# Performance work log

Measured on AMD Instinct MI355X. Metric: run time of the kernel, lower is better.

## Reference

```python
import jax, jax.numpy as jnp
import numpy as np

N, E = 50000, 800000
IN_FEAT = OUT_FEAT = 128
EMB = 3
K = 3  # k_order + 1
BN_EPS = 1e-5


def setup_inputs() -> dict:
    key = jax.random.key(0)
    ks = jax.random.split(key, 12)
    feature = jax.random.normal(ks[0], (N, IN_FEAT), jnp.float32)
    coords = jax.random.normal(ks[1], (N, EMB), jnp.float32)
    src = jax.random.randint(ks[2], (E,), 0, N, jnp.int32)
    dst = jax.random.randint(ks[3], (E,), 0, N, jnp.int32)
    order = jax.random.randint(ks[4], (E,), 0, K, jnp.int32)
    # xavier_normal_ on [K, in, out]: torch treats last two dims as (fan_in, fan_out)
    std_lin = float(np.sqrt(2.0 / (IN_FEAT + OUT_FEAT)))
    linear = jax.random.normal(ks[5], (K, IN_FEAT, OUT_FEAT), jnp.float32) * std_lin
    # attention_layer: Linear(EMB, OUT_FEAT, bias=False); store as [EMB, OUT_FEAT]
    lim_att = float(1.0 / np.sqrt(EMB))
    attW = jax.random.uniform(ks[6], (EMB, OUT_FEAT), jnp.float32, -lim_att, lim_att)
    lim_mlp = float(1.0 / np.sqrt(OUT_FEAT))
    mlp_w = jax.random.uniform(ks[7], (OUT_FEAT, OUT_FEAT), jnp.float32, -lim_mlp, lim_mlp)
    mlp_b = jax.random.uniform(ks[8], (OUT_FEAT,), jnp.float32, -lim_mlp, lim_mlp)
    bn_gamma = jnp.ones((OUT_FEAT,), jnp.float32)
    bn_beta = jnp.zeros((OUT_FEAT,), jnp.float32)
    return {"feature": feature, "coords": coords, "src": src, "dst": dst,
            "order": order, "linear": linear, "attW": attW,
            "mlp_w": mlp_w, "mlp_b": mlp_b, "bn_gamma": bn_gamma, "bn_beta": bn_beta}


def reference(feature, coords, src, dst, order, linear, attW, mlp_w, mlp_b, bn_gamma, bn_beta):
    n = feature.shape[0]
    # --- edge attention: dot(attention_layer(c_src - c_dst), h_src) ---
    dc = coords[src] - coords[dst]                      # [E, EMB]
    att = jnp.sum((dc @ attW) * feature[src], axis=1)   # [E]
    invdist = 1.0 / (jnp.sum(dc * dc, axis=1) + 1.0)    # [E], 1/(||dc||^2 + 1)
    # --- messages: per-edge weight selection linear[order] @ h_src ---
    # msg depends only on (src node, order): precompute per-order node transforms
    xk = jnp.einsum('ni,kio->kno', feature, linear)     # [K, N, OUT]
    msg = xk[order, src]                                # [E, OUT]
    # --- segment softmax over incoming edges of dst ---
    m = jax.ops.segment_max(att, dst, num_segments=n)   # [N]
    ex = jnp.exp(att - m[dst])                          # [E]
    denom = jax.ops.segment_sum(ex, dst, num_segments=n)
    d_g = denom[dst]
    alpha = ex / jnp.where(d_g > 0, d_g, 1.0)
    # --- weighted scatter-add aggregation ---
    w = (alpha * invdist)[:, None]                      # [E, 1]
    h = jax.ops.segment_sum(w * msg, dst, num_segments=n)  # [N, OUT]
    # --- mlp: Linear -> ReLU -> BatchNorm1d (training-mode batch stats) ---
    y = jax.nn.relu(h @ mlp_w.T + mlp_b)
    mean = jnp.mean(y, axis=0)
    var = jnp.var(y, axis=0)  # biased, matches torch BN normalization
    y = (y - mean) * jax.lax.rsqrt(var + BN_EPS) * bn_gamma + bn_beta
    return y
```

## Files before the change

kernel.cpp:

```cpp
#include <hip/hip_runtime.h>

#define N_NODES 50000
#define E_EDGES 800000
#define FEAT    128
#define KORD    3
#define BN_EPS  1e-5f
#define NB1     49
#define NBUK    49
#define BCAP    20480
#define NSHARD  16

typedef __fp16 f16x2 __attribute__((ext_vector_type(2)));
typedef __fp16 f16x8 __attribute__((ext_vector_type(8)));
typedef __attribute__((ext_vector_type(4))) float f32x4;

__device__ __forceinline__ unsigned h2u(f16x2 h) { union { f16x2 h; unsigned u; } c; c.h = h; return c.u; }
__device__ __forceinline__ f16x2 u2h(unsigned u) { union { unsigned u; f16x2 h; } c; c.u = u; return c.h; }

__device__ __forceinline__ void gload16(const void* g, void* l) {
    __builtin_amdgcn_global_load_lds(
        (const __attribute__((address_space(1))) unsigned int*)g,
        (__attribute__((address_space(3))) unsigned int*)l, 16, 0, 0);
}

__global__ void gprep(const float* __restrict__ W, const float* __restrict__ L,
                      __fp16* __restrict__ GT) {
    __shared__ float wrow[FEAT];
    const int o = blockIdx.x;
    const int i = threadIdx.x;
    wrow[i] = W[o * FEAT + i];
    __syncthreads();
    #pragma unroll
    for (int k = 0; k < KORD; ++k) {
        const float* lp = L + ((size_t)k * FEAT + i) * FEAT;
        float acc = 0.f;
        #pragma unroll 8
        for (int j = 0; j < FEAT; ++j) acc = fmaf(lp[j], wrow[j], acc);
        GT[(size_t)o * 384 + k * FEAT + i] = (__fp16)acc;
    }
}

__global__ void g_cast(const float* __restrict__ feat,
                       const float* __restrict__ coords,
                       const float* __restrict__ attW,
                       __fp16* __restrict__ fh,
                       float4* __restrict__ pk) {
    const int node = (blockIdx.x * blockDim.x + threadIdx.x) >> 6;
    const int lane = threadIdx.x & 63;
    if (node >= N_NODES) return;
    const float2 f = *(const float2*)(feat + (size_t)node * FEAT + lane * 2);
    *(f16x2*)(fh + (size_t)node * FEAT + lane * 2) = __builtin_amdgcn_cvt_pkrtz(f.x, f.y);
    float gg[3];
    #pragma unroll
    for (int j = 0; j < 3; ++j) {
        float p = f.x * attW[j * FEAT + lane * 2] + f.y * attW[j * FEAT + lane * 2 + 1];
        #pragma unroll
        for (int off = 32; off; off >>= 1) p += __shfl_xor(p, off);
        gg[j] = p;
    }
    if (lane == 0) {
        const float c0 = coords[node * 3 + 0], c1 = coords[node * 3 + 1], c2 = coords[node * 3 + 2];
        pk[2 * node]     = make_float4(c0, c1, c2, gg[0]);
        pk[2 * node + 1] = make_float4(gg[1], gg[2], 0.f, 0.f);
    }
}

__global__ __launch_bounds__(256)
void bucketA(const int* __restrict__ src, const int* __restrict__ dst,
             const int* __restrict__ order,
             int* __restrict__ cnt, int* __restrict__ gcur, int2* __restrict__ bbuf) {
    __shared__ int lcnt[NBUK];
    __shared__ int lbase[NBUK];
    const int tid = threadIdx.x;
    if (tid < NBUK) lcnt[tid] = 0;
    __syncthreads();
    const int e0 = blockIdx.x * 2048;
    int b[8], r[8], so[8], dd[8];
    #pragma unroll
    for (int i = 0; i < 8; ++i) {
        const int e = e0 + i * 256 + tid;
        if (e < E_EDGES) {
            dd[i] = dst[e];
            so[i] = (order[e] << 16) | src[e];
            b[i] = dd[i] >> 10;
            r[i] = atomicAdd(&lcnt[b[i]], 1);
            atomicAdd(cnt + dd[i], 1);
        } else b[i] = -1;
    }
    __syncthreads();
    if (tid < NBUK) lbase[tid] = atomicAdd(&gcur[tid], lcnt[tid]);
    __syncthreads();
    #pragma unroll
    for (int i = 0; i < 8; ++i)
        if (b[i] >= 0)
            bbuf[(size_t)b[i] * BCAP + lbase[b[i]] + r[i]] = make_int2(so[i], dd[i]);
}

__global__ __launch_bounds__(256)
void scan1(const int* __restrict__ cnt, int* __restrict__ rowptr, int* __restrict__ bsum) {
    __shared__ int lds[256];
    const int b = blockIdx.x, t = threadIdx.x;
    const int base = b * 1024 + t * 4;
    int v[4];
    #pragma unroll
    for (int i = 0; i < 4; ++i) v[i] = (base + i < N_NODES) ? cnt[base + i] : 0;
    lds[t] = v[0] + v[1] + v[2] + v[3];
    __syncthreads();
    for (int off = 1; off < 256; off <<= 1) {
        const int u = (t >= off) ? lds[t - off] : 0;
        __syncthreads();
        lds[t] += u;
        __syncthreads();
    }
    int excl = t ? lds[t - 1] : 0;
    if (t == 255) bsum[b] = lds[255];
    #pragma unroll
    for (int i = 0; i < 4; ++i) {
        if (base + i < N_NODES) rowptr[base + i] = excl;
        excl += v[i];
    }
}

__global__ void scan2(const int* __restrict__ bsum, int* __restrict__ boff,
                      int* __restrict__ rowptr) {
    const int lane = threadIdx.x;
    const int v = (lane < NB1) ? bsum[lane] : 0;
    int incl = v;
    #pragma unroll
    for (int off = 1; off < 64; off <<= 1) {
        const int u = __shfl_up(incl, off);
        if (lane >= off) incl += u;
    }
    if (lane < NB1) boff[lane] = incl - v;
    if (lane == 0) rowptr[N_NODES] = E_EDGES;
}

__global__ void scan3(int* __restrict__ rowptr, int* __restrict__ cursor,
                      const int* __restrict__ boff) {
    const int i = blockIdx.x * blockDim.x + threadIdx.x;
    if (i >= N_NODES) return;
    const int v = rowptr[i] + boff[i >> 10];
    rowptr[i] = v;
    cursor[i] = v;
}

__global__ void bucketB(const int* __restrict__ gcur, const int2* __restrict__ bbuf,
                        int* __restrict__ cursor, int* __restrict__ sord_p) {
    const int b = blockIdx.x >> 3;
    const int seg = blockIdx.x & 7;
    const int n = gcur[b];
    const int lo = (int)((long)n * seg / 8), hi = (int)((long)n * (seg + 1) / 8);
    for (int i = lo + (int)threadIdx.x; i < hi; i += 256) {
        const int2 ent = bbuf[(size_t)b * BCAP + i];
        const int pos = atomicAdd(cursor + ent.y, 1);
        sord_p[pos] = ent.x;
    }
}

__global__ void segagg(const float4* __restrict__ pk,
                       const int* __restrict__ sord_p,
                       const int* __restrict__ rowptr,
                       const __fp16* __restrict__ fh,
                       __fp16* __restrict__ agg) {
    __shared__ uint4 stash[4][72];
    const int node = (blockIdx.x * blockDim.x + threadIdx.x) >> 6;
    const int lane = threadIdx.x & 63;
    const int wid  = threadIdx.x >> 6;
    if (node >= N_NODES) return;
    const int beg = rowptr[node], end = rowptr[node + 1];
    const float4 b0 = pk[2 * node];

    if (lane < 8) stash[wid][64 + lane] = make_uint4(0u, 0u, 0u, 0u);

    float att0 = -1e30f, inv0 = 0.f; int sol0 = 0;
    float m = -1e30f, s = 0.f;
    int nch = 0;
    for (int cb = beg; cb < end; cb += 64, ++nch) {
        const int p = cb + lane;
        float a = -1e30f, iv = 0.f; int so = 0;
        if (p < end) {
            so = sord_p[p];
            const int sn = so & 0xFFFF;
            const float4 a0 = pk[2 * sn], a1 = pk[2 * sn + 1];
            const float dx = a0.x - b0.x, dy = a0.y - b0.y, dz = a0.z - b0.z;
            a = dx * a0.w + dy * a1.x + dz * a1.y;
            iv = 1.f / (dx * dx + dy * dy + dz * dz + 1.f);
        }
        if (nch == 0) { att0 = a; inv0 = iv; sol0 = so; }
        const float mn = fmaxf(m, a);
        s = s * __expf(m - mn) + ((p < end) ? __expf(a - mn) : 0.f);
        m = mn;
    }
    #pragma unroll
    for (int off = 32; off; off >>= 1) {
        const float mo = __shfl_xor(m, off), so_ = __shfl_xor(s, off);
        const float mn = fmaxf(m, mo);
        s = s * __expf(m - mn) + so_ * __expf(mo - mn);
        m = mn;
    }
    const float inv_s = s > 0.f ? 1.f / s : 0.f;

    const int grp = lane >> 4;
    const int fl  = lane & 15;
    f16x2 ac[3][4];
    #pragma unroll
    for (int o = 0; o < 3; ++o)
        #pragma unroll
        for (int q = 0; q < 4; ++q) ac[o][q] = (f16x2){0, 0};

    int ch = 0;
    for (int cb = beg; cb < end; cb += 64, ++ch) {
        const int p = cb + lane;
        float wl = 0.f; int so = 0;
        if (ch == 0) {
            wl = __expf(att0 - m) * inv_s * inv0;
            so = sol0;
        } else if (p < end) {
            so = sord_p[p];
            const int sn = so & 0xFFFF;
            const float4 a0 = pk[2 * sn], a1 = pk[2 * sn + 1];
            const float dx = a0.x - b0.x, dy = a0.y - b0.y, dz = a0.z - b0.z;
            const float a = dx * a0.w + dy * a1.x + dz * a1.y;
            wl = __expf(a - m) * inv_s / (dx * dx + dy * dy + dz * dz + 1.f);
        }
        const int k = so >> 16;
        const __fp16 wh = (__fp16)wl;
        f16x2 w2; w2.x = wh; w2.y = wh;
        const unsigned uw = h2u(w2);
        stash[wid][lane] = make_uint4(k == 0 ? uw : 0u, k == 1 ? uw : 0u,
                                      k == 2 ? uw : 0u, (unsigned)(so & 0xFFFF));
        const int ne = min(64, end - cb);
        const uint4* st = stash[wid];
        for (int t = 0; t < ne; t += 4) {
            const uint4 e = st[t + grp];
            const uint4 v = *(const uint4*)(fh + ((size_t)e.w << 7) + fl * 8);
            const f16x2 w0 = u2h(e.x), w1 = u2h(e.y), w2v = u2h(e.z);
            const f16x2 va = u2h(v.x), vb = u2h(v.y), vc = u2h(v.z), vd = u2h(v.w);
            ac[0][0] = __builtin_elementwise_fma(va, w0, ac[0][0]);
            ac[0][1] = __builtin_elementwise_fma(vb, w0, ac[0][1]);
            ac[0][2] = __builtin_elementwise_fma(vc, w0, ac[0][2]);
            ac[0][3] = __builtin_elementwise_fma(vd, w0, ac[0][3]);
            ac[1][0] = __builtin_elementwise_fma(va, w1, ac[1][0]);
            ac[1][1] = __builtin_elementwise_fma(vb, w1, ac[1][1]);
            ac[1][2] = __builtin_elementwise_fma(vc, w1, ac[1][2]);
            ac[1][3] = __builtin_elementwise_fma(vd, w1, ac[1][3]);
            ac[2][0] = __builtin_elementwise_fma(va, w2v, ac[2][0]);
            ac[2][1] = __builtin_elementwise_fma(vb, w2v, ac[2][1]);
            ac[2][2] = __builtin_elementwise_fma(vc, w2v, ac[2][2]);
            ac[2][3] = __builtin_elementwise_fma(vd, w2v, ac[2][3]);
        }
    }
    #pragma unroll
    for (int o = 0; o < 3; ++o)
        #pragma unroll
        for (int q = 0; q < 4; ++q) {
            ac[o][q] = ac[o][q] + u2h(__shfl_xor((int)h2u(ac[o][q]), 16));
            ac[o][q] = ac[o][q] + u2h(__shfl_xor((int)h2u(ac[o][q]), 32));
        }
    if (lane < 16) {
        __fp16* row = agg + (size_t)node * 384 + fl * 8;
        *(uint4*)(row)       = make_uint4(h2u(ac[0][0]), h2u(ac[0][1]), h2u(ac[0][2]), h2u(ac[0][3]));
        *(uint4*)(row + 128) = make_uint4(h2u(ac[1][0]), h2u(ac[1][1]), h2u(ac[1][2]), h2u(ac[1][3]));
        *(uint4*)(row + 256) = make_uint4(h2u(ac[2][0]), h2u(ac[2][1]), h2u(ac[2][2]), h2u(ac[2][3]));
    }
}

__global__ __launch_bounds__(256)
void mlp_gemm(const __fp16* __restrict__ agg, const __fp16* __restrict__ GT,
              float* __restrict__ out, int M,
              const float* __restrict__ bias, float* __restrict__ sbuf) {
    __shared__ char smem[49152];
    const int m0 = blockIdx.x * 64;
    const int tid = threadIdx.x;
    const int wave = tid >> 6, lane = tid & 63;
    const int wm0 = wave * 16;
    const int lrow = lane & 15;
    const int kg = lane >> 4;
    const int srow = lane >> 3;
    const int schunk = lane & 7;

    auto STAGE = [&](int buf, int kc) {
        char* base = smem + buf * 24576;
        #pragma unroll
        for (int j = 0; j < 2; ++j) {
            const int rl = wave * 16 + j * 8 + srow;
            const int rg = min(m0 + rl, M - 1);
            gload16(agg + (size_t)rg * 384 + kc * 64 + ((schunk ^ (rl & 7)) << 3),
                    base + (wave * 16 + j * 8) * 128);
        }
        #pragma unroll
        for (int j = 0; j < 4; ++j) {
            const int rl = wave * 32 + j * 8 + srow;
            gload16(GT + (size_t)rl * 384 + kc * 64 + ((schunk ^ (rl & 7)) << 3),
                    base + 8192 + (wave * 32 + j * 8) * 128);
        }
    };

    f32x4 acc[8];
    #pragma unroll
    for (int b = 0; b < 8; ++b) acc[b] = (f32x4){0.f, 0.f, 0.f, 0.f};

    STAGE(0, 0);
    __syncthreads();

    for (int kc = 0; kc < 6; ++kc) {
        const int buf = kc & 1;
        if (kc < 5) STAGE(buf ^ 1, kc + 1);
        const char* Ab = smem + buf * 24576;
        const char* Bb = Ab + 8192;
        f16x8 afr[2];
        #pragma unroll
        for (int ks = 0; ks < 2; ++ks) {
            const int row = wm0 + lrow;
            afr[ks] = *(const f16x8*)(Ab + row * 128 + (((ks * 4 + kg) ^ (row & 7)) << 4));
        }
        #pragma unroll
        for (int nf = 0; nf < 8; ++nf) {
            #pragma unroll
            for (int ks = 0; ks < 2; ++ks) {
                const int row = nf * 16 + lrow;
                f16x8 bfr = *(const f16x8*)(Bb + row * 128 + (((ks * 4 + kg) ^ (row & 7)) << 4));
                acc[nf] = __builtin_amdgcn_mfma_f32_16x16x32_f16(afr[ks], bfr, acc[nf], 0, 0, 0);
            }
        }
        __syncthreads();
    }

    float s[8], s2[8], bv[8];
    #pragma unroll
    for (int nf = 0; nf < 8; ++nf) { s[nf] = 0.f; s2[nf] = 0.f; bv[nf] = bias[nf * 16 + lrow]; }
    #pragma unroll
    for (int nf = 0; nf < 8; ++nf)
        #pragma unroll
        for (int rg = 0; rg < 4; ++rg) {
            const int row = m0 + wm0 + kg * 4 + rg;
            if (row < M) {
                const float v = fmaxf(acc[nf][rg] + bv[nf], 0.f);
                out[(size_t)row * FEAT + nf * 16 + lrow] = v;
                s[nf] += v;
                s2[nf] = fmaf(v, v, s2[nf]);
            }
        }
    #pragma unroll
    for (int nf = 0; nf < 8; ++nf) {
        s[nf]  += __shfl_xor(s[nf], 16);  s[nf]  += __shfl_xor(s[nf], 32);
        s2[nf] += __shfl_xor(s2[nf], 16); s2[nf] += __shfl_xor(s2[nf], 32);
    }
    __syncthreads();
    float* red = (float*)smem;
    if (lane < 16) {
        #pragma unroll
        for (int nf = 0; nf < 8; ++nf) {
            red[wave * 256 + nf * 16 + lane]       = s[nf];
            red[wave * 256 + 128 + nf * 16 + lane] = s2[nf];
        }
    }
    __syncthreads();
    if (tid < 128) {
        const float ss = red[tid] + red[256 + tid] + red[512 + tid] + red[768 + tid];
        const float qq = red[128 + tid] + red[384 + tid] + red[640 + tid] + red[896 + tid];
        float* sb = sbuf + (blockIdx.x & (NSHARD - 1)) * 256;
        atomicAdd(sb + tid, ss);
        atomicAdd(sb + FEAT + tid, qq);
    }
}

__global__ void normalize(float* __restrict__ y, const float* __restrict__ sbuf,
                          const float* __restrict__ gamma, const float* __restrict__ beta) {
    __shared__ float sc_s[FEAT], sh_s[FEAT];
    const int t = threadIdx.x;
    if (t < FEAT) {
        float ssum = 0.f, qsum = 0.f;
        #pragma unroll
        for (int sh = 0; sh < NSHARD; ++sh) {
            ssum += sbuf[sh * 256 + t];
            qsum += sbuf[sh * 256 + 128 + t];
        }
        const float mean = ssum / (float)N_NODES;
        const float var  = qsum / (float)N_NODES - mean * mean;
        const float sc   = gamma[t] * rsqrtf(var + BN_EPS);
        sc_s[t] = sc;
        sh_s[t] = beta[t] - mean * sc;
    }
    __syncthreads();
    const int idx = blockIdx.x * blockDim.x + t;
    const int o4 = (idx & 31) * 4;
    float4 v = *(float4*)(y + (size_t)idx * 4);
    const float4 sc = *(const float4*)(sc_s + o4);
    const float4 sh = *(const float4*)(sh_s + o4);
    v.x = fmaf(v.x, sc.x, sh.x);
    v.y = fmaf(v.y, sc.y, sh.y);
    v.z = fmaf(v.z, sc.z, sh.z);
    v.w = fmaf(v.w, sc.w, sh.w);
    *(float4*)(y + (size_t)idx * 4) = v;
}

extern "C" void kernel_launch(void* const* d_in, const int* in_sizes, int n_in,
                              void* d_out, int out_size, void* d_ws, size_t ws_size,
                              hipStream_t stream) {
    const float* feature = (const float*)d_in[0];
    const float* coords  = (const float*)d_in[1];
    const int*   src     = (const int*)d_in[2];
    const int*   dst     = (const int*)d_in[3];
    const int*   order   = (const int*)d_in[4];
    const float* linear  = (const float*)d_in[5];
    const float* attW    = (const float*)d_in[6];
    const float* mlp_w   = (const float*)d_in[7];
    const float* mlp_b   = (const float*)d_in[8];
    const float* gamma   = (const float*)d_in[9];
    const float* beta    = (const float*)d_in[10];
    float* out = (float*)d_out;

    char* p = (char*)d_ws;
    __fp16* fh           = (__fp16*)p;  p += (size_t)N_NODES * FEAT * 2;
    __fp16* agg          = (__fp16*)p;  p += (size_t)N_NODES * 384 * 2;
    __fp16* GT           = (__fp16*)p;  p += (size_t)FEAT * 384 * 2;
    float4* pk           = (float4*)p;  p += (size_t)N_NODES * 32;
    int*   sord_p        = (int*)p;     p += (size_t)E_EDGES * 4;
    int2*  bbuf          = (int2*)p;    p += (size_t)NBUK * BCAP * 8;
    int*   cnt           = (int*)p;     p += 200064;
    float* sbuf          = (float*)p;   p += NSHARD * 256 * 4;
    int*   gcur          = (int*)p;     p += 1024;
    int*   rowptr        = (int*)p;     p += 200064;
    int*   cursor        = (int*)p;     p += 200064;
    int*   bsum          = (int*)p;     p += 256;
    int*   boff          = (int*)p;     p += 256;

    hipMemsetAsync(cnt, 0, 200064 + NSHARD * 256 * 4 + 1024, stream);

    const int NWB = (N_NODES * 64) / 256;
    const int MB  = (N_NODES + 63) / 64;
    const int AB  = (E_EDGES + 2047) / 2048;

    gprep<<<FEAT, FEAT, 0, stream>>>(mlp_w, linear, GT);
    g_cast<<<NWB, 256, 0, stream>>>(feature, coords, attW, fh, pk);

    bucketA<<<AB, 256, 0, stream>>>(src, dst, order, cnt, gcur, bbuf);
    scan1<<<NB1, 256, 0, stream>>>(cnt, rowptr, bsum);
    scan2<<<1, 64, 0, stream>>>(bsum, boff, rowptr);
    scan3<<<(N_NODES + 255) / 256, 256, 0, stream>>>(rowptr, cursor, boff);
    bucketB<<<NBUK * 8, 256, 0, stream>>>(gcur, bbuf, cursor, sord_p);

    segagg<<<NWB, 256, 0, stream>>>(pk, sord_p, rowptr, fh, agg);

    mlp_gemm<<<MB, 256, 0, stream>>>(agg, GT, out, N_NODES, mlp_b, sbuf);
    normalize<<<(N_NODES * 32) / 256, 256, 0, stream>>>(out, sbuf, gamma, beta);
}
```

Measured before the change: 186.2 us.

## Precompute edge attention in bucket scatter, merge prep kernels, unroll gather loop

Moves the per-edge attention score and inverse-distance calculation from segagg into bucketB, which writes them to new CSR-ordered arrays att_p/invd_p. segagg then reads them contiguously instead of gathering node records twice. The gprep kernel is folded into extra blocks of g_cast, scan2 is folded into scan3 (each block recomputes the 49-entry prefix), and the feature-gather loop is unrolled by two to keep more loads in flight. This cuts two kernel launches and repeated random pk gathers, at the cost of extra global writes and reads of two 800K-float arrays and random-position scatter stores.

```diff
diff --git a/kernel.cpp b/kernel.cpp
--- a/kernel.cpp
+++ b/kernel.cpp
@@ -9,6 +9,7 @@
 #define NBUK    49
 #define BCAP    20480
 #define NSHARD  16
+#define NWB_BLKS 12500
 
 typedef __fp16 f16x2 __attribute__((ext_vector_type(2)));
 typedef __fp16 f16x8 __attribute__((ext_vector_type(8)));
@@ -23,28 +24,32 @@
         (__attribute__((address_space(3))) unsigned int*)l, 16, 0, 0);
 }
 
-__global__ void gprep(const float* __restrict__ W, const float* __restrict__ L,
-                      __fp16* __restrict__ GT) {
-    __shared__ float wrow[FEAT];
-    const int o = blockIdx.x;
-    const int i = threadIdx.x;
-    wrow[i] = W[o * FEAT + i];
-    __syncthreads();
-    #pragma unroll
-    for (int k = 0; k < KORD; ++k) {
-        const float* lp = L + ((size_t)k * FEAT + i) * FEAT;
-        float acc = 0.f;
-        #pragma unroll 8
-        for (int j = 0; j < FEAT; ++j) acc = fmaf(lp[j], wrow[j], acc);
-        GT[(size_t)o * 384 + k * FEAT + i] = (__fp16)acc;
-    }
-}
-
 __global__ void g_cast(const float* __restrict__ feat,
                        const float* __restrict__ coords,
                        const float* __restrict__ attW,
+                       const float* __restrict__ W,
+                       const float* __restrict__ L,
                        __fp16* __restrict__ fh,
-                       float4* __restrict__ pk) {
+                       float4* __restrict__ pk,
+                       __fp16* __restrict__ GT) {
+    __shared__ float wrow[FEAT];
+    if (blockIdx.x >= NWB_BLKS) {
+        const int o = blockIdx.x - NWB_BLKS;
+        const int i = threadIdx.x;
+        if (i < FEAT) wrow[i] = W[o * FEAT + i];
+        __syncthreads();
+        if (i < FEAT) {
+            #pragma unroll
+            for (int k = 0; k < KORD; ++k) {
+                const float* lp = L + ((size_t)k * FEAT + i) * FEAT;
+                float acc = 0.f;
+                #pragma unroll 8
+                for (int j = 0; j < FEAT; ++j) acc = fmaf(lp[j], wrow[j], acc);
+                GT[(size_t)o * 384 + k * FEAT + i] = (__fp16)acc;
+            }
+        }
+        return;
+    }
     const int node = (blockIdx.x * blockDim.x + threadIdx.x) >> 6;
     const int lane = threadIdx.x & 63;
     if (node >= N_NODES) return;
@@ -121,72 +126,73 @@
     }
 }
 
-__global__ void scan2(const int* __restrict__ bsum, int* __restrict__ boff,
-                      int* __restrict__ rowptr) {
-    const int lane = threadIdx.x;
-    const int v = (lane < NB1) ? bsum[lane] : 0;
-    int incl = v;
-    #pragma unroll
-    for (int off = 1; off < 64; off <<= 1) {
-        const int u = __shfl_up(incl, off);
-        if (lane >= off) incl += u;
-    }
-    if (lane < NB1) boff[lane] = incl - v;
-    if (lane == 0) rowptr[N_NODES] = E_EDGES;
-}
-
 __global__ void scan3(int* __restrict__ rowptr, int* __restrict__ cursor,
-                      const int* __restrict__ boff) {
-    const int i = blockIdx.x * blockDim.x + threadIdx.x;
-    if (i >= N_NODES) return;
-    const int v = rowptr[i] + boff[i >> 10];
-    rowptr[i] = v;
-    cursor[i] = v;
+                      const int* __restrict__ bsum) {
+    __shared__ int boff_s[64];
+    const int t = threadIdx.x;
+    if (t < 64) {
+        const int v = (t < NB1) ? bsum[t] : 0;
+        int incl = v;
+        #pragma unroll
+        for (int off = 1; off < 64; off <<= 1) {
+            const int u = __shfl_up(incl, off);
+            if (t >= off) incl += u;
+        }
+        boff_s[t] = incl - v;
+    }
+    __syncthreads();
+    const int i = blockIdx.x * 256 + t;
+    if (i < N_NODES) {
+        const int v = rowptr[i] + boff_s[i >> 10];
+        rowptr[i] = v;
+        cursor[i] = v;
+    }
+    if (i == 0) rowptr[N_NODES] = E_EDGES;
 }
 
 __global__ void bucketB(const int* __restrict__ gcur, const int2* __restrict__ bbuf,
-                        int* __restrict__ cursor, int* __restrict__ sord_p) {
+                        const float4* __restrict__ pk,
+                        int* __restrict__ cursor, int* __restrict__ sord_p,
+                        float* __restrict__ att_p, float* __restrict__ invd_p) {
     const int b = blockIdx.x >> 3;
     const int seg = blockIdx.x & 7;
     const int n = gcur[b];
     const int lo = (int)((long)n * seg / 8), hi = (int)((long)n * (seg + 1) / 8);
     for (int i = lo + (int)threadIdx.x; i < hi; i += 256) {
         const int2 ent = bbuf[(size_t)b * BCAP + i];
-        const int pos = atomicAdd(cursor + ent.y, 1);
+        const int s = ent.x & 0xFFFF;
+        const int d = ent.y;
+        const float4 a0 = pk[2 * s], a1 = pk[2 * s + 1], c0 = pk[2 * d];
+        const float dx = a0.x - c0.x, dy = a0.y - c0.y, dz = a0.z - c0.z;
+        const float att  = dx * a0.w + dy * a1.x + dz * a1.y;
+        const float invd = 1.f / (dx * dx + dy * dy + dz * dz + 1.f);
+        const int pos = atomicAdd(cursor + d, 1);
         sord_p[pos] = ent.x;
-    }
-}
-
-__global__ void segagg(const float4* __restrict__ pk,
-                       const int* __restrict__ sord_p,
+        att_p[pos]  = att;
+        invd_p[pos] = invd;
+    }
+}
+
+__global__ void segagg(const int* __restrict__ sord_p,
+                       const float* __restrict__ att_p,
+                       const float* __restrict__ invd_p,
                        const int* __restrict__ rowptr,
                        const __fp16* __restrict__ fh,
                        __fp16* __restrict__ agg) {
-    __shared__ uint4 stash[4][72];
+    __shared__ uint4 stash[4][64];
     const int node = (blockIdx.x * blockDim.x + threadIdx.x) >> 6;
     const int lane = threadIdx.x & 63;
     const int wid  = threadIdx.x >> 6;
     if (node >= N_NODES) return;
     const int beg = rowptr[node], end = rowptr[node + 1];
-    const float4 b0 = pk[2 * node];
-
-    if (lane < 8) stash[wid][64 + lane] = make_uint4(0u, 0u, 0u, 0u);
-
-    float att0 = -1e30f, inv0 = 0.f; int sol0 = 0;
+
+    float a0c = -1e30f;
     float m = -1e30f, s = 0.f;
     int nch = 0;
     for (int cb = beg; cb < end; cb += 64, ++nch) {
         const int p = cb + lane;
-        float a = -1e30f, iv = 0.f; int so = 0;
-        if (p < end) {
-            so = sord_p[p];
-            const int sn = so & 0xFFFF;
-            const float4 a0 = pk[2 * sn], a1 = pk[2 * sn + 1];
-            const float dx = a0.x - b0.x, dy = a0.y - b0.y, dz = a0.z - b0.z;
-            a = dx * a0.w + dy * a1.x + dz * a1.y;
-            iv = 1.f / (dx * dx + dy * dy + dz * dz + 1.f);
-        }
-        if (nch == 0) { att0 = a; inv0 = iv; sol0 = so; }
+        const float a = (p < end) ? att_p[p] : -1e30f;
+        if (nch == 0) a0c = a;
         const float mn = fmaxf(m, a);
         s = s * __expf(m - mn) + ((p < end) ? __expf(a - mn) : 0.f);
         m = mn;
@@ -212,16 +218,10 @@
     for (int cb = beg; cb < end; cb += 64, ++ch) {
         const int p = cb + lane;
         float wl = 0.f; int so = 0;
-        if (ch == 0) {
-            wl = __expf(att0 - m) * inv_s * inv0;
-            so = sol0;
-        } else if (p < end) {
+        if (p < end) {
+            const float a = (ch == 0) ? a0c : att_p[p];
+            wl = __expf(a - m) * inv_s * invd_p[p];
             so = sord_p[p];
-            const int sn = so & 0xFFFF;
-            const float4 a0 = pk[2 * sn], a1 = pk[2 * sn + 1];
-            const float dx = a0.x - b0.x, dy = a0.y - b0.y, dz = a0.z - b0.z;
-            const float a = dx * a0.w + dy * a1.x + dz * a1.y;
-            wl = __expf(a - m) * inv_s / (dx * dx + dy * dy + dz * dz + 1.f);
         }
         const int k = so >> 16;
         const __fp16 wh = (__fp16)wl;
@@ -231,23 +231,43 @@
                                       k == 2 ? uw : 0u, (unsigned)(so & 0xFFFF));
         const int ne = min(64, end - cb);
         const uint4* st = stash[wid];
-        for (int t = 0; t < ne; t += 4) {
-            const uint4 e = st[t + grp];
-            const uint4 v = *(const uint4*)(fh + ((size_t)e.w << 7) + fl * 8);
-            const f16x2 w0 = u2h(e.x), w1 = u2h(e.y), w2v = u2h(e.z);
-            const f16x2 va = u2h(v.x), vb = u2h(v.y), vc = u2h(v.z), vd = u2h(v.w);
-            ac[0][0] = __builtin_elementwise_fma(va, w0, ac[0][0]);
-            ac[0][1] = __builtin_elementwise_fma(vb, w0, ac[0][1]);
-            ac[0][2] = __builtin_elementwise_fma(vc, w0, ac[0][2]);
-            ac[0][3] = __builtin_elementwise_fma(vd, w0, ac[0][3]);
-            ac[1][0] = __builtin_elementwise_fma(va, w1, ac[1][0]);
-            ac[1][1] = __builtin_elementwise_fma(vb, w1, ac[1][1]);
-            ac[1][2] = __builtin_elementwise_fma(vc, w1, ac[1][2]);
-            ac[1][3] = __builtin_elementwise_fma(vd, w1, ac[1][3]);
-            ac[2][0] = __builtin_elementwise_fma(va, w2v, ac[2][0]);
-            ac[2][1] = __builtin_elementwise_fma(vb, w2v, ac[2][1]);
-            ac[2][2] = __builtin_elementwise_fma(vc, w2v, ac[2][2]);
-            ac[2][3] = __builtin_elementwise_fma(vd, w2v, ac[2][3]);
+        for (int t = 0; t < ne; t += 8) {
+            const uint4 e1 = st[t + grp];
+            const uint4 e2 = st[t + 4 + grp];
+            const uint4 v1 = *(const uint4*)(fh + ((size_t)e1.w << 7) + fl * 8);
+            const uint4 v2 = *(const uint4*)(fh + ((size_t)e2.w << 7) + fl * 8);
+            {
+                const f16x2 w0 = u2h(e1.x), w1 = u2h(e1.y), w2v = u2h(e1.z);
+                const f16x2 va = u2h(v1.x), vb = u2h(v1.y), vc = u2h(v1.z), vd = u2h(v1.w);
+                ac[0][0] = __builtin_elementwise_fma(va, w0, ac[0][0]);
+                ac[0][1] = __builtin_elementwise_fma(vb, w0, ac[0][1]);
+                ac[0][2] = __builtin_elementwise_fma(vc, w0, ac[0][2]);
+                ac[0][3] = __builtin_elementwise_fma(vd, w0, ac[0][3]);
+                ac[1][0] = __builtin_elementwise_fma(va, w1, ac[1][0]);
+                ac[1][1] = __builtin_elementwise_fma(vb, w1, ac[1][1]);
+                ac[1][2] = __builtin_elementwise_fma(vc, w1, ac[1][2]);
+                ac[1][3] = __builtin_elementwise_fma(vd, w1, ac[1][3]);
+                ac[2][0] = __builtin_elementwise_fma(va, w2v, ac[2][0]);
+                ac[2][1] = __builtin_elementwise_fma(vb, w2v, ac[2][1]);
+                ac[2][2] = __builtin_elementwise_fma(vc, w2v, ac[2][2]);
+                ac[2][3] = __builtin_elementwise_fma(vd, w2v, ac[2][3]);
+            }
+            {
+                const f16x2 w0 = u2h(e2.x), w1 = u2h(e2.y), w2v = u2h(e2.z);
+                const f16x2 va = u2h(v2.x), vb = u2h(v2.y), vc = u2h(v2.z), vd = u2h(v2.w);
+                ac[0][0] = __builtin_elementwise_fma(va, w0, ac[0][0]);
+                ac[0][1] = __builtin_elementwise_fma(vb, w0, ac[0][1]);
+                ac[0][2] = __builtin_elementwise_fma(vc, w0, ac[0][2]);
+                ac[0][3] = __builtin_elementwise_fma(vd, w0, ac[0][3]);
+                ac[1][0] = __builtin_elementwise_fma(va, w1, ac[1][0]);
+                ac[1][1] = __builtin_elementwise_fma(vb, w1, ac[1][1]);
+                ac[1][2] = __builtin_elementwise_fma(vc, w1, ac[1][2]);
+                ac[1][3] = __builtin_elementwise_fma(vd, w1, ac[1][3]);
+                ac[2][0] = __builtin_elementwise_fma(va, w2v, ac[2][0]);
+                ac[2][1] = __builtin_elementwise_fma(vb, w2v, ac[2][1]);
+                ac[2][2] = __builtin_elementwise_fma(vc, w2v, ac[2][2]);
+                ac[2][3] = __builtin_elementwise_fma(vd, w2v, ac[2][3]);
+            }
         }
     }
     #pragma unroll
@@ -417,6 +437,8 @@
     __fp16* GT           = (__fp16*)p;  p += (size_t)FEAT * 384 * 2;
     float4* pk           = (float4*)p;  p += (size_t)N_NODES * 32;
     int*   sord_p        = (int*)p;     p += (size_t)E_EDGES * 4;
+    float* att_p         = (float*)p;   p += (size_t)E_EDGES * 4;
+    float* invd_p        = (float*)p;   p += (size_t)E_EDGES * 4;
     int2*  bbuf          = (int2*)p;    p += (size_t)NBUK * BCAP * 8;
     int*   cnt           = (int*)p;     p += 200064;
     float* sbuf          = (float*)p;   p += NSHARD * 256 * 4;
@@ -424,24 +446,21 @@
     int*   rowptr        = (int*)p;     p += 200064;
     int*   cursor        = (int*)p;     p += 200064;
     int*   bsum          = (int*)p;     p += 256;
-    int*   boff          = (int*)p;     p += 256;
 
     hipMemsetAsync(cnt, 0, 200064 + NSHARD * 256 * 4 + 1024, stream);
 
-    const int NWB = (N_NODES * 64) / 256;
-    const int MB  = (N_NODES + 63) / 64;
-    const int AB  = (E_EDGES + 2047) / 2048;
-
-    gprep<<<FEAT, FEAT, 0, stream>>>(mlp_w, linear, GT);
-    g_cast<<<NWB, 256, 0, stream>>>(feature, coords, attW, fh, pk);
+    const int MB = (N_NODES + 63) / 64;
+    const int AB = (E_EDGES + 2047) / 2048;
+
+    g_cast<<<NWB_BLKS + FEAT, 256, 0, stream>>>(feature, coords, attW,
+                                                mlp_w, linear, fh, pk, GT);
 
     bucketA<<<AB, 256, 0, stream>>>(src, dst, order, cnt, gcur, bbuf);
     scan1<<<NB1, 256, 0, stream>>>(cnt, rowptr, bsum);
-    scan2<<<1, 64, 0, stream>>>(bsum, boff, rowptr);
-    scan3<<<(N_NODES + 255) / 256, 256, 0, stream>>>(rowptr, cursor, boff);
-    bucketB<<<NBUK * 8, 256, 0, stream>>>(gcur, bbuf, cursor, sord_p);
-
-    segagg<<<NWB, 256, 0, stream>>>(pk, sord_p, rowptr, fh, agg);
+    scan3<<<(N_NODES + 255) / 256, 256, 0, stream>>>(rowptr, cursor, bsum);
+    bucketB<<<NBUK * 8, 256, 0, stream>>>(gcur, bbuf, pk, cursor, sord_p, att_p, invd_p);
+
+    segagg<<<NWB_BLKS, 256, 0, stream>>>(sord_p, att_p, invd_p, rowptr, fh, agg);
 
     mlp_gemm<<<MB, 256, 0, stream>>>(agg, GT, out, N_NODES, mlp_b, sbuf);
     normalize<<<(N_NODES * 32) / 256, 256, 0, stream>>>(out, sbuf, gamma, beta);
```

Result: slower. 191.6 us (+2.9%).
